# Optimization experiments

Hardware: AMD Instinct MI355X
Metric: run time of the kernel (lower is better)

## Reference

```python
import jax, jax.numpy as jnp
import numpy as np

IN_C, OUT_C, K, N_FILTERS, STRIDE, PAD = 256, 512, 3, 64, 1, 1


def setup_inputs() -> dict:
    key = jax.random.key(0)
    kx, kw, kb, krw, krb = jax.random.split(key, 5)
    fan_in = IN_C * K * K
    bound = 1.0 / np.sqrt(fan_in)
    x = jax.random.normal(kx, (32, IN_C, 56, 56), dtype=jnp.float32)
    weight = jax.random.uniform(kw, (OUT_C, IN_C, K, K), minval=-bound, maxval=bound, dtype=jnp.float32)
    bias = jax.random.uniform(kb, (OUT_C,), minval=-bound, maxval=bound, dtype=jnp.float32)
    rbound = 1.0 / np.sqrt(IN_C)
    router_w = jax.random.uniform(krw, (OUT_C, IN_C), minval=-rbound, maxval=rbound, dtype=jnp.float32)
    router_b = jax.random.uniform(krb, (OUT_C,), minval=-rbound, maxval=rbound, dtype=jnp.float32)
    return {"x": x, "weight": weight, "bias": bias, "router_w": router_w, "router_b": router_b}


def reference(x, weight, bias, router_w, router_b):
    B = x.shape[0]
    # router: global avg pool -> linear -> top-k channel mask
    pooled = jnp.mean(x, axis=(2, 3))                      # [B, IN_C]
    router_out = pooled @ router_w.T + router_b            # [B, OUT_C]
    _, top_idx = jax.lax.top_k(router_out, N_FILTERS)      # [B, k]
    mask = jnp.zeros((B, OUT_C), dtype=x.dtype).at[jnp.arange(B)[:, None], top_idx].set(1.0)
    # dense conv2d
    conv = jax.lax.conv_general_dilated(
        x, weight, window_strides=(STRIDE, STRIDE), padding=[(PAD, PAD), (PAD, PAD)],
        dimension_numbers=("NCHW", "OIHW", "NCHW"))
    conv = conv + bias[None, :, None, None]
    return conv * mask[:, :, None, None]
```

## Files before the change

kernel.cpp:

```cpp
#include <hip/hip_runtime.h>

#define IN_C   256
#define OUT_C  512
#define WIDTH  56
#define HW     3136
#define KTOT   2304
#define NF     64
#define NB     32
#define NGRP   8
#define TN     128
#define NTILE  25
#define XROWS  242
#define LDX    40

typedef __bf16 bf16x8 __attribute__((ext_vector_type(8)));
typedef float  f32x4  __attribute__((ext_vector_type(4)));

__global__ __launch_bounds__(256) void pool_kernel(const float* __restrict__ x,
                                                   float* __restrict__ pooled) {
    int bc = blockIdx.x;
    const float* src = x + (size_t)bc * HW;
    float s = 0.f;
    for (int i = threadIdx.x; i < HW; i += 256) s += src[i];
    #pragma unroll
    for (int off = 32; off > 0; off >>= 1) s += __shfl_down(s, off, 64);
    __shared__ float wsum[4];
    int lane = threadIdx.x & 63, wv = threadIdx.x >> 6;
    if (lane == 0) wsum[wv] = s;
    __syncthreads();
    if (threadIdx.x == 0)
        pooled[bc] = (wsum[0] + wsum[1] + wsum[2] + wsum[3]) * (1.0f / HW);
}

__global__ __launch_bounds__(512) void router_kernel(const float* __restrict__ pooled,
                                                     const float* __restrict__ rw,
                                                     const float* __restrict__ rb,
                                                     int* __restrict__ sel,
                                                     int* __restrict__ selflag) {
    int b = blockIdx.x;
    __shared__ float p[IN_C];
    __shared__ float v[OUT_C];
    __shared__ int   scount;
    int t = threadIdx.x;
    if (t < IN_C) p[t] = pooled[b * IN_C + t];
    if (t == 0) scount = 0;
    __syncthreads();
    float acc = rb[t];
    const float* wrow = rw + (size_t)t * IN_C;
    for (int i = 0; i < IN_C; ++i) acc += p[i] * wrow[i];
    v[t] = acc;
    __syncthreads();
    int cnt = 0;
    for (int j = 0; j < OUT_C; ++j) {
        float o = v[j];
        cnt += (o > acc) || (o == acc && j < t);
    }
    int is_sel = (cnt < NF) ? 1 : 0;
    selflag[b * OUT_C + t] = is_sel;
    if (is_sel) {
        int pos = atomicAdd(&scount, 1);
        sel[b * NF + pos] = t;
    }
}

__global__ __launch_bounds__(256) void compact_w(const float* __restrict__ w,
                                                 const int* __restrict__ sel,
                                                 __bf16* __restrict__ Acomp) {
    int id = blockIdx.x;
    int b = id / 72, rem = id - b * 72;
    int g = rem / 9, tap = rem - g * 9;
    int t = threadIdx.x;
    int oc = t >> 2, q = t & 3;
    int s = sel[b * NF + oc];
    const float* wsrc = w + (size_t)s * KTOT + tap;
    bf16x8 o;
    #pragma unroll
    for (int j = 0; j < 8; ++j)
        o[j] = (__bf16)wsrc[(g * 32 + q * 8 + j) * 9];
    *(bf16x8*)&Acomp[((size_t)id * 64 + oc) * 32 + q * 8] = o;
}

__global__ __launch_bounds__(256) void zero_unselected(const int* __restrict__ selflag,
                                                       float* __restrict__ out) {
    int bc = blockIdx.x;
    if (selflag[bc]) return;
    float4* dst = (float4*)(out + (size_t)bc * HW);
    float4 z = {0.f, 0.f, 0.f, 0.f};
    for (int i = threadIdx.x; i < HW / 4; i += 256) dst[i] = z;
}

__global__ __launch_bounds__(256, 4) void conv_kernel(const float* __restrict__ x,
                                                      const __bf16* __restrict__ Acomp,
                                                      const float* __restrict__ bias,
                                                      const int* __restrict__ sel,
                                                      float* __restrict__ out) {
    int b     = blockIdx.y;
    int ptile = blockIdx.x * TN;
    int t     = threadIdx.x;
    int lane  = t & 63, wv = t >> 6;
    int fm    = lane & 15, fq = lane >> 4;
    int m_base = (wv & 1) * 32;
    int n_base = (wv >> 1) * 64;

    __shared__ __bf16 xlds[2][XROWS * LDX];

    const float*  x_b    = x + (size_t)b * IN_C * HW;
    const __bf16* a_base = Acomp + (size_t)b * (NGRP * 9 * 64 * 32);

    int pp[4], poh[4], pow_[4];
    #pragma unroll
    for (int s = 0; s < 4; ++s) {
        int p = ptile + n_base + s * 16 + fm;
        pp[s] = p;
        int pc = p < HW ? p : HW - 1;
        poh[s]  = pc / WIDTH;
        pow_[s] = pc - poh[s] * WIDTH;
    }

    int  sp   = t;
    bool sact = sp < XROWS;
    int  gp   = ptile - 57 + sp;
    gp = gp < 0 ? 0 : (gp > HW - 1 ? HW - 1 : gp);
    const float* sx = x_b + gp;

    if (sact) {
        #pragma unroll
        for (int oct = 0; oct < 4; ++oct) {
            float v[8];
            #pragma unroll
            for (int j = 0; j < 8; ++j) v[j] = sx[(size_t)(oct * 8 + j) * HW];
            bf16x8 o;
            #pragma unroll
            for (int j = 0; j < 8; ++j) o[j] = (__bf16)v[j];
            *(bf16x8*)&xlds[0][sp * LDX + oct * 8] = o;
        }
    }
    __syncthreads();

    f32x4 acc[2][4] = {};
    float pre[32];

    for (int g = 0; g < NGRP; ++g) {
        int cur = g & 1;
        if (g < NGRP - 1 && sact) {
            #pragma unroll
            for (int i = 0; i < 32; ++i)
                pre[i] = sx[(size_t)((g + 1) * 32 + i) * HW];
        }
        const __bf16* ap = a_base + (size_t)g * 9 * 64 * 32;
        #pragma unroll
        for (int t9 = 0; t9 < 9; ++t9) {
            const int r = t9 / 3, c = t9 - 3 * (t9 / 3);
            const int shift = (r - 1) * WIDTH + (c - 1);
            bf16x8 af0 = *(const bf16x8*)(ap + ((size_t)(t9 * 64 + m_base + fm)) * 32 + fq * 8);
            bf16x8 af1 = *(const bf16x8*)(ap + ((size_t)(t9 * 64 + m_base + 16 + fm)) * 32 + fq * 8);
            #pragma unroll
            for (int s = 0; s < 4; ++s) {
                int ohr = poh[s] + r - 1, owc = pow_[s] + c - 1;
                bool ok = ((unsigned)ohr < 56u) && ((unsigned)owc < 56u);
                int n = n_base + s * 16 + fm;
                bf16x8 bfr = *(const bf16x8*)&xlds[cur][(n + 57 + shift) * LDX + fq * 8];
                bf16x8 z = {};
                bfr = ok ? bfr : z;
                acc[0][s] = __builtin_amdgcn_mfma_f32_16x16x32_bf16(af0, bfr, acc[0][s], 0, 0, 0);
                acc[1][s] = __builtin_amdgcn_mfma_f32_16x16x32_bf16(af1, bfr, acc[1][s], 0, 0, 0);
            }
        }
        if (g < NGRP - 1) {
            if (sact) {
                #pragma unroll
                for (int oct = 0; oct < 4; ++oct) {
                    bf16x8 o;
                    #pragma unroll
                    for (int j = 0; j < 8; ++j) o[j] = (__bf16)pre[oct * 8 + j];
                    *(bf16x8*)&xlds[cur ^ 1][sp * LDX + oct * 8] = o;
                }
            }
            __syncthreads();
        }
    }

    const int* selb = sel + b * NF;
    size_t outb = (size_t)b * OUT_C * HW;
    #pragma unroll
    for (int i = 0; i < 2; ++i) {
        #pragma unroll
        for (int reg = 0; reg < 4; ++reg) {
            int m  = m_base + i * 16 + fq * 4 + reg;
            int oc = selb[m];
            float bs = bias[oc];
            float* orow = out + outb + (size_t)oc * HW;
            #pragma unroll
            for (int s = 0; s < 4; ++s)
                if (pp[s] < HW) orow[pp[s]] = acc[i][s][reg] + bs;
        }
    }
}

extern "C" void kernel_launch(void* const* d_in, const int* in_sizes, int n_in,
                              void* d_out, int out_size, void* d_ws, size_t ws_size,
                              hipStream_t stream) {
    (void)in_sizes; (void)n_in; (void)ws_size; (void)out_size;
    const float* x        = (const float*)d_in[0];
    const float* weight   = (const float*)d_in[1];
    const float* bias     = (const float*)d_in[2];
    const float* router_w = (const float*)d_in[3];
    const float* router_b = (const float*)d_in[4];
    float* out = (float*)d_out;

    char* ws = (char*)d_ws;
    float*  pooled  = (float*)ws;
    int*    sel     = (int*)(ws + 32768);
    int*    selflag = (int*)(ws + 40960);
    __bf16* Acomp   = (__bf16*)(ws + 131072);

    pool_kernel<<<NB * IN_C, 256, 0, stream>>>(x, pooled);
    router_kernel<<<NB, OUT_C, 0, stream>>>(pooled, router_w, router_b, sel, selflag);
    compact_w<<<NB * NGRP * 9, 256, 0, stream>>>(weight, sel, Acomp);
    zero_unselected<<<NB * OUT_C, 256, 0, stream>>>(selflag, out);

    dim3 grid(NTILE, NB);
    conv_kernel<<<grid, 256, 0, stream>>>(x, Acomp, bias, sel, out);
}
```

Before: 405.5 us.

## Fuse unselected-channel zeroing into conv kernel and retile waves by M

```diff
diff --git a/kernel.cpp b/kernel.cpp
--- a/kernel.cpp
+++ b/kernel.cpp
@@ -6,6 +6,7 @@
 #define HW     3136
 #define KTOT   2304
 #define NF     64
+#define NU     448
 #define NB     32
 #define NGRP   8
 #define TN     128
@@ -36,14 +37,14 @@
                                                      const float* __restrict__ rw,
                                                      const float* __restrict__ rb,
                                                      int* __restrict__ sel,
-                                                     int* __restrict__ selflag) {
+                                                     int* __restrict__ unsel) {
     int b = blockIdx.x;
     __shared__ float p[IN_C];
     __shared__ float v[OUT_C];
-    __shared__ int   scount;
+    __shared__ int   scount, ucount;
     int t = threadIdx.x;
     if (t < IN_C) p[t] = pooled[b * IN_C + t];
-    if (t == 0) scount = 0;
+    if (t == 0) { scount = 0; ucount = 0; }
     __syncthreads();
     float acc = rb[t];
     const float* wrow = rw + (size_t)t * IN_C;
@@ -55,11 +56,12 @@
         float o = v[j];
         cnt += (o > acc) || (o == acc && j < t);
     }
-    int is_sel = (cnt < NF) ? 1 : 0;
-    selflag[b * OUT_C + t] = is_sel;
-    if (is_sel) {
+    if (cnt < NF) {
         int pos = atomicAdd(&scount, 1);
         sel[b * NF + pos] = t;
+    } else {
+        int pos = atomicAdd(&ucount, 1);
+        unsel[b * NU + pos] = t;
     }
 }
 
@@ -80,36 +82,32 @@
     *(bf16x8*)&Acomp[((size_t)id * 64 + oc) * 32 + q * 8] = o;
 }
 
-__global__ __launch_bounds__(256) void zero_unselected(const int* __restrict__ selflag,
-                                                       float* __restrict__ out) {
-    int bc = blockIdx.x;
-    if (selflag[bc]) return;
-    float4* dst = (float4*)(out + (size_t)bc * HW);
-    float4 z = {0.f, 0.f, 0.f, 0.f};
-    for (int i = threadIdx.x; i < HW / 4; i += 256) dst[i] = z;
-}
-
 __global__ __launch_bounds__(256, 4) void conv_kernel(const float* __restrict__ x,
                                                       const __bf16* __restrict__ Acomp,
                                                       const float* __restrict__ bias,
                                                       const int* __restrict__ sel,
+                                                      const int* __restrict__ unsel,
                                                       float* __restrict__ out) {
-    int b     = blockIdx.y;
-    int ptile = blockIdx.x * TN;
-    int t     = threadIdx.x;
-    int lane  = t & 63, wv = t >> 6;
-    int fm    = lane & 15, fq = lane >> 4;
-    int m_base = (wv & 1) * 32;
-    int n_base = (wv >> 1) * 64;
+    int id   = blockIdx.x;
+    int xcd  = id & 7, slot = id >> 3;
+    int bq   = slot / NTILE;
+    int tile = slot - bq * NTILE;
+    int b    = xcd * 4 + bq;
+    int ptile = tile * TN;
+
+    int t    = threadIdx.x;
+    int lane = t & 63, wv = t >> 6;
+    int fm   = lane & 15, fq = lane >> 4;
+    int n_base = wv * 32;
 
     __shared__ __bf16 xlds[2][XROWS * LDX];
 
     const float*  x_b    = x + (size_t)b * IN_C * HW;
     const __bf16* a_base = Acomp + (size_t)b * (NGRP * 9 * 64 * 32);
 
-    int pp[4], poh[4], pow_[4];
-    #pragma unroll
-    for (int s = 0; s < 4; ++s) {
+    int pp[2], poh[2], pow_[2];
+    #pragma unroll
+    for (int s = 0; s < 2; ++s) {
         int p = ptile + n_base + s * 16 + fm;
         pp[s] = p;
         int pc = p < HW ? p : HW - 1;
@@ -137,7 +135,7 @@
     }
     __syncthreads();
 
-    f32x4 acc[2][4] = {};
+    f32x4 acc[4][2] = {};
     float pre[32];
 
     for (int g = 0; g < NGRP; ++g) {
@@ -147,23 +145,27 @@
             for (int i = 0; i < 32; ++i)
                 pre[i] = sx[(size_t)((g + 1) * 32 + i) * HW];
         }
-        const __bf16* ap = a_base + (size_t)g * 9 * 64 * 32;
+        const __bf16* gp_a = a_base + (size_t)g * 9 * 64 * 32;
         #pragma unroll
         for (int t9 = 0; t9 < 9; ++t9) {
             const int r = t9 / 3, c = t9 - 3 * (t9 / 3);
             const int shift = (r - 1) * WIDTH + (c - 1);
-            bf16x8 af0 = *(const bf16x8*)(ap + ((size_t)(t9 * 64 + m_base + fm)) * 32 + fq * 8);
-            bf16x8 af1 = *(const bf16x8*)(ap + ((size_t)(t9 * 64 + m_base + 16 + fm)) * 32 + fq * 8);
-            #pragma unroll
-            for (int s = 0; s < 4; ++s) {
+            const __bf16* ap = gp_a + (size_t)t9 * 64 * 32;
+            bf16x8 af[4];
+            #pragma unroll
+            for (int mi = 0; mi < 4; ++mi)
+                af[mi] = *(const bf16x8*)(ap + (size_t)(mi * 16 + fm) * 32 + fq * 8);
+            #pragma unroll
+            for (int s = 0; s < 2; ++s) {
                 int ohr = poh[s] + r - 1, owc = pow_[s] + c - 1;
                 bool ok = ((unsigned)ohr < 56u) && ((unsigned)owc < 56u);
                 int n = n_base + s * 16 + fm;
                 bf16x8 bfr = *(const bf16x8*)&xlds[cur][(n + 57 + shift) * LDX + fq * 8];
                 bf16x8 z = {};
                 bfr = ok ? bfr : z;
-                acc[0][s] = __builtin_amdgcn_mfma_f32_16x16x32_bf16(af0, bfr, acc[0][s], 0, 0, 0);
-                acc[1][s] = __builtin_amdgcn_mfma_f32_16x16x32_bf16(af1, bfr, acc[1][s], 0, 0, 0);
+                #pragma unroll
+                for (int mi = 0; mi < 4; ++mi)
+                    acc[mi][s] = __builtin_amdgcn_mfma_f32_16x16x32_bf16(af[mi], bfr, acc[mi][s], 0, 0, 0);
             }
         }
         if (g < NGRP - 1) {
@@ -183,16 +185,28 @@
     const int* selb = sel + b * NF;
     size_t outb = (size_t)b * OUT_C * HW;
     #pragma unroll
-    for (int i = 0; i < 2; ++i) {
+    for (int mi = 0; mi < 4; ++mi) {
         #pragma unroll
         for (int reg = 0; reg < 4; ++reg) {
-            int m  = m_base + i * 16 + fq * 4 + reg;
+            int m  = mi * 16 + fq * 4 + reg;
             int oc = selb[m];
             float bs = bias[oc];
             float* orow = out + outb + (size_t)oc * HW;
             #pragma unroll
-            for (int s = 0; s < 4; ++s)
-                if (pp[s] < HW) orow[pp[s]] = acc[i][s][reg] + bs;
+            for (int s = 0; s < 2; ++s)
+                if (pp[s] < HW) orow[pp[s]] = acc[mi][s][reg] + bs;
+        }
+    }
+
+    {
+        const int* unselb = unsel + b * NU;
+        int j = t & 31;
+        bool jok = (ptile + j * 4) < HW;
+        float4 z = {0.f, 0.f, 0.f, 0.f};
+        for (int u = t >> 5; u < NU; u += 8) {
+            int oc = unselb[u];
+            if (jok)
+                *(float4*)(out + outb + (size_t)oc * HW + ptile + j * 4) = z;
         }
     }
 }
@@ -209,16 +223,14 @@
     float* out = (float*)d_out;
 
     char* ws = (char*)d_ws;
-    float*  pooled  = (float*)ws;
-    int*    sel     = (int*)(ws + 32768);
-    int*    selflag = (int*)(ws + 40960);
-    __bf16* Acomp   = (__bf16*)(ws + 131072);
+    float*  pooled = (float*)ws;
+    int*    sel    = (int*)(ws + 32768);
+    int*    unsel  = (int*)(ws + 40960);
+    __bf16* Acomp  = (__bf16*)(ws + 131072);
 
     pool_kernel<<<NB * IN_C, 256, 0, stream>>>(x, pooled);
-    router_kernel<<<NB, OUT_C, 0, stream>>>(pooled, router_w, router_b, sel, selflag);
+    router_kernel<<<NB, OUT_C, 0, stream>>>(pooled, router_w, router_b, sel, unsel);
     compact_w<<<NB * NGRP * 9, 256, 0, stream>>>(weight, sel, Acomp);
-    zero_unselected<<<NB * OUT_C, 256, 0, stream>>>(selflag, out);
-
-    dim3 grid(NTILE, NB);
-    conv_kernel<<<grid, 256, 0, stream>>>(x, Acomp, bias, sel, out);
-}
+
+    conv_kernel<<<NTILE * NB, 256, 0, stream>>>(x, Acomp, bias, sel, unsel, out);
+}
```

After: 406.3 us. About the same (+0.2%).
